# Kernel tuning notes

Measured on AMD Instinct MI355X. Metric: run time of the kernel, lower is better.

## Reference

```python
import jax, jax.numpy as jnp
import numpy as np

N = 100000   # nodes
E = 1600000  # edges
DIN, DH, DOUT = 128, 64, 40
EPS = 1e-5


def setup_inputs() -> dict:
    key = jax.random.key(0)
    ks = jax.random.split(key, 16)
    glorot = lambda k, shp: jax.random.normal(k, shp, jnp.float32) / np.float32(np.sqrt(shp[0]))
    return {
        'x': jax.random.normal(ks[0], (N, DIN), jnp.float32),
        'edge_index': jax.random.randint(ks[1], (2, E), 0, N, jnp.int64),
        'W0': glorot(ks[2], (DIN, DH)), 'b0': jnp.zeros((DH,), jnp.float32),
        'W1': glorot(ks[3], (DH, DH)),  'b1': jnp.zeros((DH,), jnp.float32),
        'W2': glorot(ks[4], (DH, DH)),  'b2': jnp.zeros((DH,), jnp.float32),
        'ln0_g': jnp.ones((DH,), jnp.float32), 'ln0_b': jnp.zeros((DH,), jnp.float32),
        'ln1_g': jnp.ones((DH,), jnp.float32), 'ln1_b': jnp.zeros((DH,), jnp.float32),
        'mpW0': glorot(ks[5], (DH, DH)),  'mpb0': jnp.zeros((DH,), jnp.float32),
        'mpW1': glorot(ks[6], (DH, DOUT)), 'mpb1': jnp.zeros((DOUT,), jnp.float32),
    }


def _layernorm(h, g, b):
    mu = jnp.mean(h, axis=-1, keepdims=True)
    var = jnp.mean(jnp.square(h - mu), axis=-1, keepdims=True)
    return (h - mu) * jax.lax.rsqrt(var + EPS) * g + b


def _gcn_conv(x, src, dst, norm_e, self_w, W, b):
    # PyG GCNConv: h = x W; out = sum_{(s,d)} norm * h[s] scattered to d,
    # plus self-loop term, plus bias.  norm = d^{-1/2}[s] * d^{-1/2}[d] on A+I.
    h = x @ W                                        # [N, out]
    agg = jnp.zeros_like(h).at[dst].add(h[src] * norm_e[:, None])
    agg = agg + h * self_w[:, None]                  # self loops (i,i)
    return agg + b


def reference(x, edge_index, W0, b0, W1, b1, W2, b2,
              ln0_g, ln0_b, ln1_g, ln1_b, mpW0, mpb0, mpW1, mpb1):
    src, dst = edge_index[0], edge_index[1]
    # degree on A + I (count incoming edges at dst, +1 for self loop)
    deg = jnp.zeros((N,), jnp.float32).at[dst].add(1.0) + 1.0
    dinv = jax.lax.rsqrt(deg)
    norm_e = dinv[src] * dinv[dst]                   # per-edge weight [E]
    self_w = dinv * dinv                             # self-loop weight [N]

    h = x
    convs = [(W0, b0), (W1, b1), (W2, b2)]
    lns = [(ln0_g, ln0_b), (ln1_g, ln1_b)]
    for i, (W, b) in enumerate(convs):
        h = _gcn_conv(h, src, dst, norm_e, self_w, W, b)
        h = jax.nn.relu(h)
        # dropout: training=False -> identity
        if i != len(convs) - 1:
            g, bb = lns[i]
            h = _layernorm(h, g, bb)

    # post_mp: Linear -> Dropout(identity) -> Linear
    h = h @ mpW0 + mpb0
    return h @ mpW1 + mpb1
```

## Files before the change

kernel.cpp:

```cpp
#include <hip/hip_runtime.h>
#include <hip/hip_bf16.h>

#define NN 100000
#define EE 1600000
#define DOUT 40
#define LN_EPS 1e-5f
#define NBUCK 391
#define TILE 2048
#define TBLK 782
#define BCAP 8192

typedef __attribute__((ext_vector_type(8))) short short8;
typedef __attribute__((ext_vector_type(4))) float f32x4;

__device__ __forceinline__ float blo(unsigned u) { return __uint_as_float(u << 16); }
__device__ __forceinline__ float bhi(unsigned u) { return __uint_as_float(u & 0xffff0000u); }
__device__ __forceinline__ unsigned bpack(float lo, float hi) {
    unsigned a = __float_as_uint(lo);
    unsigned b = __float_as_uint(hi);
    a = (a + 0x7fffu + ((a >> 16) & 1u)) >> 16;
    b = (b + 0x7fffu + ((b >> 16) & 1u)) & 0xffff0000u;
    return (a & 0xffffu) | b;
}

__global__ void binit_k(int* __restrict__ bucketCur) {
    int b = blockIdx.x * 256 + threadIdx.x;
    if (b < NBUCK) bucketCur[b] = b * BCAP;
}

__global__ __launch_bounds__(512, 8) void bucket_k(const int* __restrict__ src,
                                                   const int* __restrict__ dst,
                                                   int* __restrict__ bucketCur,
                                                   unsigned* __restrict__ bE) {
    __shared__ int cnt[8][NBUCK];
    __shared__ int basew[8][NBUCK];
    int tid = threadIdx.x;
    int wv = tid >> 6;
    for (int i = tid; i < 8 * NBUCK; i += 512) ((int*)cnt)[i] = 0;
    __syncthreads();
    long e0 = (long)blockIdx.x * TILE;
    int d[4];
#pragma unroll
    for (int i = 0; i < 4; ++i) {
        long e = e0 + tid + i * 512;
        d[i] = (e < EE) ? dst[e] : -1;
    }
#pragma unroll
    for (int i = 0; i < 4; ++i) {
        if (d[i] >= 0) atomicAdd(&cnt[wv][d[i] >> 8], 1);
    }
    __syncthreads();
    for (int b = tid; b < NBUCK; b += 512) {
        int c[8];
        int tot = 0;
#pragma unroll
        for (int w = 0; w < 8; ++w) { c[w] = cnt[w][b]; tot += c[w]; }
        int base = tot ? atomicAdd(&bucketCur[b], tot) : 0;
        int run = base;
#pragma unroll
        for (int w = 0; w < 8; ++w) { basew[w][b] = run; run += c[w]; cnt[w][b] = 0; }
    }
    __syncthreads();
#pragma unroll
    for (int i = 0; i < 4; ++i) {
        if (d[i] >= 0) {
            long e = e0 + tid + i * 512;
            int b = d[i] >> 8;
            int pos = basew[wv][b] + atomicAdd(&cnt[wv][b], 1);
            bE[pos] = (unsigned)src[e] | ((unsigned)(d[i] & 255) << 24);
        }
    }
}

__global__ __launch_bounds__(512, 4) void reorder2_k(const int* __restrict__ bucketCur,
                                                     const unsigned* __restrict__ bE,
                                                     int* __restrict__ csrSrc,
                                                     int* __restrict__ degI,
                                                     int* __restrict__ cursor,
                                                     float* __restrict__ dinv) {
    __shared__ int sScan[512];
    __shared__ int sHist[256];
    __shared__ int sPre[256];
    __shared__ int sStart[256];
    int tid = threadIdx.x;
    int b = blockIdx.x;
    int c = (tid < NBUCK) ? (bucketCur[tid] - tid * BCAP) : 0;
    sScan[tid] = c;
    __syncthreads();
    for (int off = 1; off < 512; off <<= 1) {
        int t = (tid >= off) ? sScan[tid - off] : 0;
        __syncthreads();
        sScan[tid] += t;
        __syncthreads();
    }
    int bbase = (b == 0) ? 0 : sScan[b - 1];
    if (tid < 256) sHist[tid] = 0;
    __syncthreads();
    int start = b * BCAP;
    int end = bucketCur[b];
    for (int e = start + tid; e < end; e += 512) {
        unsigned v = bE[e];
        atomicAdd(&sHist[v >> 24], 1);
    }
    __syncthreads();
    if (tid < 256) sPre[tid] = sHist[tid];
    __syncthreads();
    for (int off = 1; off < 256; off <<= 1) {
        int t = (tid >= off && tid < 256) ? sPre[tid - off] : 0;
        __syncthreads();
        if (tid < 256) sPre[tid] += t;
        __syncthreads();
    }
    if (tid < 256) {
        int h = sHist[tid];
        int excl = sPre[tid] - h;
        int st = bbase + excl;
        sStart[tid] = st;
        int nd = (b << 8) + tid;
        if (nd < NN) {
            degI[nd] = h;
            cursor[nd] = st;
            dinv[nd] = rsqrtf((float)h + 1.0f);
        }
    }
    __syncthreads();
    for (int e = start + tid; e < end; e += 512) {
        unsigned v = bE[e];
        int pos = atomicAdd(&sStart[v >> 24], 1);
        csrSrc[pos] = (int)(v & 0xFFFFFFu);
    }
}

template <int K>
__global__ __launch_bounds__(256, 2) void gemm_mfma(const float* __restrict__ X,
                                                    const float* __restrict__ W,
                                                    const float* __restrict__ dinv,
                                                    unsigned* __restrict__ H) {
    constexpr int C = K / 32;
    __shared__ unsigned short sW16[K * 66];
    __shared__ float sD[64 * 65];
    int tid = threadIdx.x;
    for (int i = tid; i < K * 64; i += 256) {
        int k = i >> 6, n = i & 63;
        sW16[k * 66 + n] = (unsigned short)(bpack(W[i], 0.f) & 0xffffu);
    }
    __syncthreads();
    int wv = tid >> 6, lane = tid & 63;
    int q = lane >> 4, ln = lane & 15;
    short8 bfrag[C][4];
#pragma unroll
    for (int c = 0; c < C; ++c) {
#pragma unroll
        for (int t = 0; t < 4; ++t) {
            int kb = (c * 32 + q * 8) * 66 + t * 16 + ln;
            unsigned u0 = (unsigned)sW16[kb]       | ((unsigned)sW16[kb + 66]  << 16);
            unsigned u1 = (unsigned)sW16[kb + 132] | ((unsigned)sW16[kb + 198] << 16);
            unsigned u2 = (unsigned)sW16[kb + 264] | ((unsigned)sW16[kb + 330] << 16);
            unsigned u3 = (unsigned)sW16[kb + 396] | ((unsigned)sW16[kb + 462] << 16);
            uint4 u = make_uint4(u0, u1, u2, u3);
            bfrag[c][t] = __builtin_bit_cast(short8, u);
        }
    }
    int base = blockIdx.x * 64;
    int node = base + wv * 16 + ln;
    bool ok = node < NN;
    short8 afrag[C];
#pragma unroll
    for (int c = 0; c < C; ++c) {
        float4 f0 = make_float4(0.f, 0.f, 0.f, 0.f);
        float4 f1 = make_float4(0.f, 0.f, 0.f, 0.f);
        if (ok) {
            const float4* xp = (const float4*)(X + (long)node * K + c * 32 + q * 8);
            f0 = xp[0];
            f1 = xp[1];
        }
        uint4 u;
        u.x = bpack(f0.x, f0.y);
        u.y = bpack(f0.z, f0.w);
        u.z = bpack(f1.x, f1.y);
        u.w = bpack(f1.z, f1.w);
        afrag[c] = __builtin_bit_cast(short8, u);
    }
#pragma unroll
    for (int t = 0; t < 4; ++t) {
        f32x4 acc = {0.f, 0.f, 0.f, 0.f};
#pragma unroll
        for (int c = 0; c < C; ++c)
            acc = __builtin_amdgcn_mfma_f32_16x16x32_bf16(afrag[c], bfrag[c][t], acc, 0, 0, 0);
#pragma unroll
        for (int r = 0; r < 4; ++r)
            sD[(wv * 16 + q * 4 + r) * 65 + t * 16 + ln] = acc[r];
    }
    __syncthreads();
    for (int i = tid; i < 64 * 32; i += 256) {
        int row = i >> 5, c2 = i & 31;
        int nd = base + row;
        if (nd < NN) {
            float di = dinv[nd];
            float lo = sD[row * 65 + c2 * 2] * di;
            float hi = sD[row * 65 + c2 * 2 + 1] * di;
            H[nd * 32 + c2] = bpack(lo, hi);
        }
    }
}

__global__ __launch_bounds__(256, 2) void gemm_b(const uint4* __restrict__ Hin4,
                                                 const float* __restrict__ W,
                                                 const float* __restrict__ dinv,
                                                 unsigned* __restrict__ H) {
    __shared__ unsigned short sW16[64 * 66];
    __shared__ float sD[64 * 65];
    int tid = threadIdx.x;
    for (int i = tid; i < 64 * 64; i += 256) {
        int k = i >> 6, n = i & 63;
        sW16[k * 66 + n] = (unsigned short)(bpack(W[i], 0.f) & 0xffffu);
    }
    __syncthreads();
    int wv = tid >> 6, lane = tid & 63;
    int q = lane >> 4, ln = lane & 15;
    short8 bfrag[2][4];
#pragma unroll
    for (int c = 0; c < 2; ++c) {
#pragma unroll
        for (int t = 0; t < 4; ++t) {
            int kb = (c * 32 + q * 8) * 66 + t * 16 + ln;
            unsigned u0 = (unsigned)sW16[kb]       | ((unsigned)sW16[kb + 66]  << 16);
            unsigned u1 = (unsigned)sW16[kb + 132] | ((unsigned)sW16[kb + 198] << 16);
            unsigned u2 = (unsigned)sW16[kb + 264] | ((unsigned)sW16[kb + 330] << 16);
            unsigned u3 = (unsigned)sW16[kb + 396] | ((unsigned)sW16[kb + 462] << 16);
            uint4 u = make_uint4(u0, u1, u2, u3);
            bfrag[c][t] = __builtin_bit_cast(short8, u);
        }
    }
    int base = blockIdx.x * 64;
    int node = base + wv * 16 + ln;
    bool ok = node < NN;
    short8 afrag[2];
    {
        uint4 u0 = make_uint4(0u, 0u, 0u, 0u), u1 = u0;
        if (ok) {
            u0 = Hin4[(unsigned)node * 8u + (unsigned)q];
            u1 = Hin4[(unsigned)node * 8u + 4u + (unsigned)q];
        }
        afrag[0] = __builtin_bit_cast(short8, u0);
        afrag[1] = __builtin_bit_cast(short8, u1);
    }
#pragma unroll
    for (int t = 0; t < 4; ++t) {
        f32x4 acc = {0.f, 0.f, 0.f, 0.f};
        acc = __builtin_amdgcn_mfma_f32_16x16x32_bf16(afrag[0], bfrag[0][t], acc, 0, 0, 0);
        acc = __builtin_amdgcn_mfma_f32_16x16x32_bf16(afrag[1], bfrag[1][t], acc, 0, 0, 0);
#pragma unroll
        for (int r = 0; r < 4; ++r)
            sD[(wv * 16 + q * 4 + r) * 65 + t * 16 + ln] = acc[r];
    }
    __syncthreads();
    for (int i = tid; i < 64 * 32; i += 256) {
        int row = i >> 5, c2 = i & 31;
        int nd = base + row;
        if (nd < NN) {
            float di = dinv[nd];
            float lo = sD[row * 65 + c2 * 2] * di;
            float hi = sD[row * 65 + c2 * 2 + 1] * di;
            H[nd * 32 + c2] = bpack(lo, hi);
        }
    }
}

__global__ __launch_bounds__(256, 4) void agg_k(
        const int* __restrict__ cursor, const int* __restrict__ degI,
        const int* __restrict__ csrSrc, const float* __restrict__ dinv,
        const uint2* __restrict__ H2, const float4* __restrict__ bias4,
        const float4* __restrict__ g4, const float4* __restrict__ beta4,
        uint2* __restrict__ OUT2, int doLN) {
    int tid = threadIdx.x;
    int w = tid >> 6, lane = tid & 63;
    int g = lane >> 4;
    unsigned f = (unsigned)(lane & 15);
    unsigned node = (unsigned)(blockIdx.x * 4 + w);
    int start = cursor[node];
    int deg = degI[node];
    int myIdx = 0;
    if (lane < deg) myIdx = csrSrc[(unsigned)(start + lane)];
    float ax = 0.f, ay = 0.f, az = 0.f, aw = 0.f;
    float bx = 0.f, by = 0.f, bz = 0.f, bw = 0.f;
    uint2 q[8];
#pragma unroll
    for (int r = 0; r < 8; ++r) {
        int e = r * 4 + g;
        unsigned s = (unsigned)__shfl(myIdx, e);
        q[r] = make_uint2(0u, 0u);
        if (e < deg) q[r] = H2[s * 16u + f];
    }
#pragma unroll
    for (int r = 0; r < 8; r += 2) {
        ax += blo(q[r].x);     ay += bhi(q[r].x);
        az += blo(q[r].y);     aw += bhi(q[r].y);
        bx += blo(q[r + 1].x); by += bhi(q[r + 1].x);
        bz += blo(q[r + 1].y); bw += bhi(q[r + 1].y);
    }
    if (deg > 32) {
        int R2 = (deg + 3) >> 2;
        if (R2 > 16) R2 = 16;
        for (int r = 8; r < R2; ++r) {
            int e = r * 4 + g;
            unsigned s = (unsigned)__shfl(myIdx, e);
            uint2 qq = make_uint2(0u, 0u);
            if (e < deg) qq = H2[s * 16u + f];
            ax += blo(qq.x); ay += bhi(qq.x); az += blo(qq.y); aw += bhi(qq.y);
        }
        for (int ee = 64 + g; ee < deg; ee += 4) {
            uint2 qq = H2[(unsigned)csrSrc[(unsigned)(start + ee)] * 16u + f];
            ax += blo(qq.x); ay += bhi(qq.x); az += blo(qq.y); aw += bhi(qq.y);
        }
    }
    ax += bx; ay += by; az += bz; aw += bw;
    ax += __shfl_xor(ax, 16); ay += __shfl_xor(ay, 16);
    az += __shfl_xor(az, 16); aw += __shfl_xor(aw, 16);
    ax += __shfl_xor(ax, 32); ay += __shfl_xor(ay, 32);
    az += __shfl_xor(az, 32); aw += __shfl_xor(aw, 32);
    float di = dinv[node];
    uint2 qs = H2[node * 16u + f];
    float4 bb = bias4[f];
    float vx = fmaxf((ax + blo(qs.x)) * di + bb.x, 0.f);
    float vy = fmaxf((ay + bhi(qs.x)) * di + bb.y, 0.f);
    float vz = fmaxf((az + blo(qs.y)) * di + bb.z, 0.f);
    float vw = fmaxf((aw + bhi(qs.y)) * di + bb.w, 0.f);
    if (doLN) {
        float s = vx + vy + vz + vw;
        s += __shfl_xor(s, 1); s += __shfl_xor(s, 2);
        s += __shfl_xor(s, 4); s += __shfl_xor(s, 8);
        float mu = s * (1.f / 64.f);
        vx -= mu; vy -= mu; vz -= mu; vw -= mu;
        float vs = vx * vx + vy * vy + vz * vz + vw * vw;
        vs += __shfl_xor(vs, 1); vs += __shfl_xor(vs, 2);
        vs += __shfl_xor(vs, 4); vs += __shfl_xor(vs, 8);
        float inv = rsqrtf(vs * (1.f / 64.f) + LN_EPS);
        float4 gg = g4[f];
        float4 tt = beta4[f];
        vx = vx * inv * gg.x + tt.x;
        vy = vy * inv * gg.y + tt.y;
        vz = vz * inv * gg.z + tt.z;
        vw = vw * inv * gg.w + tt.w;
    }
    if (g == 0) OUT2[node * 16u + f] = make_uint2(bpack(vx, vy), bpack(vz, vw));
}

__global__ void fuse_k(const float* __restrict__ W0, const float* __restrict__ b0,
                       const float* __restrict__ W1, const float* __restrict__ b1,
                       float* __restrict__ Wf, float* __restrict__ bf) {
    int tid = threadIdx.x;
    for (int i = tid; i < 64 * 48; i += 256) {
        int k = i / 48, n = i % 48;
        float acc = 0.f;
        if (n < DOUT) {
            for (int j = 0; j < 64; ++j) acc = fmaf(W0[k * 64 + j], W1[j * DOUT + n], acc);
        }
        Wf[i] = acc;
    }
    for (int n = tid; n < 48; n += 256) {
        float acc = 0.f;
        if (n < DOUT) {
            acc = b1[n];
            for (int j = 0; j < 64; ++j) acc = fmaf(b0[j], W1[j * DOUT + n], acc);
        }
        bf[n] = acc;
    }
}

__global__ __launch_bounds__(256, 2) void mlp_mfma(const uint4* __restrict__ Hin4,
                                                   const float* __restrict__ Wf,
                                                   const float* __restrict__ bf,
                                                   float* __restrict__ OUT) {
    __shared__ unsigned short sW16[64 * 50];
    int tid = threadIdx.x;
    for (int i = tid; i < 64 * 48; i += 256) {
        int k = i / 48, n = i % 48;
        sW16[k * 50 + n] = (unsigned short)(bpack(Wf[i], 0.f) & 0xffffu);
    }
    __syncthreads();
    int wv = tid >> 6, lane = tid & 63;
    int q = lane >> 4, ln = lane & 15;
    short8 bfrag[2][3];
#pragma unroll
    for (int c = 0; c < 2; ++c) {
#pragma unroll
        for (int t = 0; t < 3; ++t) {
            int kb = (c * 32 + q * 8) * 50 + t * 16 + ln;
            unsigned u0 = (unsigned)sW16[kb]       | ((unsigned)sW16[kb + 50]  << 16);
            unsigned u1 = (unsigned)sW16[kb + 100] | ((unsigned)sW16[kb + 150] << 16);
            unsigned u2 = (unsigned)sW16[kb + 200] | ((unsigned)sW16[kb + 250] << 16);
            unsigned u3 = (unsigned)sW16[kb + 300] | ((unsigned)sW16[kb + 350] << 16);
            uint4 u = make_uint4(u0, u1, u2, u3);
            bfrag[c][t] = __builtin_bit_cast(short8, u);
        }
    }
    int base = blockIdx.x * 64;
    int node = base + wv * 16 + ln;
    bool ok = node < NN;
    short8 afrag[2];
    {
        uint4 u0 = make_uint4(0u, 0u, 0u, 0u), u1 = u0;
        if (ok) {
            u0 = Hin4[(unsigned)node * 8u + (unsigned)q];
            u1 = Hin4[(unsigned)node * 8u + 4u + (unsigned)q];
        }
        afrag[0] = __builtin_bit_cast(short8, u0);
        afrag[1] = __builtin_bit_cast(short8, u1);
    }
#pragma unroll
    for (int t = 0; t < 3; ++t) {
        f32x4 acc = {0.f, 0.f, 0.f, 0.f};
        acc = __builtin_amdgcn_mfma_f32_16x16x32_bf16(afrag[0], bfrag[0][t], acc, 0, 0, 0);
        acc = __builtin_amdgcn_mfma_f32_16x16x32_bf16(afrag[1], bfrag[1][t], acc, 0, 0, 0);
        int col = t * 16 + ln;
        if (col < DOUT) {
            float bv = bf[col];
#pragma unroll
            for (int r = 0; r < 4; ++r) {
                int nd = base + wv * 16 + q * 4 + r;
                if (nd < NN) OUT[(long)nd * DOUT + col] = acc[r] + bv;
            }
        }
    }
}

extern "C" void kernel_launch(void* const* d_in, const int* in_sizes, int n_in,
                              void* d_out, int out_size, void* d_ws, size_t ws_size,
                              hipStream_t stream) {
    const float* x    = (const float*)d_in[0];
    const int*   ei   = (const int*)d_in[1];
    const int*   srcI = ei;
    const int*   dstI = ei + EE;
    const float* W0   = (const float*)d_in[2];
    const float* b0   = (const float*)d_in[3];
    const float* W1   = (const float*)d_in[4];
    const float* b1   = (const float*)d_in[5];
    const float* W2   = (const float*)d_in[6];
    const float* b2   = (const float*)d_in[7];
    const float* ln0g = (const float*)d_in[8];
    const float* ln0b = (const float*)d_in[9];
    const float* ln1g = (const float*)d_in[10];
    const float* ln1b = (const float*)d_in[11];
    const float* mpW0 = (const float*)d_in[12];
    const float* mpb0 = (const float*)d_in[13];
    const float* mpW1 = (const float*)d_in[14];
    const float* mpb1 = (const float*)d_in[15];
    float* out = (float*)d_out;

    char* ws = (char*)d_ws;
    float*    dinv      = (float*)   (ws + 0);
    int*      degI      = (int*)     (ws + 512l * 1024);
    int*      cursor    = (int*)     (ws + 1024l * 1024);
    int*      bucketCur = (int*)     (ws + 1600l * 1024);
    float*    Wf        = (float*)   (ws + 1792l * 1024);
    float*    bfv       = (float*)   (ws + 1984l * 1024);
    unsigned* bE        = (unsigned*)(ws + 2048l * 1024);
    int*      csrSrc    = (int*)     (ws + 15l * 1024 * 1024);
    unsigned* bufA      = (unsigned*)(ws + 22l * 1024 * 1024);
    unsigned* bufB      = (unsigned*)(ws + 36l * 1024 * 1024);

    const int aggBlocks  = NN / 4;
    const int gemmBlocks = (NN + 63) / 64;

    binit_k<<<2, 256, 0, stream>>>(bucketCur);
    bucket_k<<<TBLK, 512, 0, stream>>>(srcI, dstI, bucketCur, bE);
    reorder2_k<<<NBUCK, 512, 0, stream>>>(bucketCur, bE, csrSrc, degI, cursor, dinv);
    fuse_k<<<1, 256, 0, stream>>>(mpW0, mpb0, mpW1, mpb1, Wf, bfv);

    gemm_mfma<128><<<gemmBlocks, 256, 0, stream>>>(x, W0, dinv, bufA);
    agg_k<<<aggBlocks, 256, 0, stream>>>(cursor, degI, csrSrc, dinv, (const uint2*)bufA,
                                         (const float4*)b0, (const float4*)ln0g,
                                         (const float4*)ln0b, (uint2*)bufB, 1);
    gemm_b<<<gemmBlocks, 256, 0, stream>>>((const uint4*)bufB, W1, dinv, bufA);
    agg_k<<<aggBlocks, 256, 0, stream>>>(cursor, degI, csrSrc, dinv, (const uint2*)bufA,
                                         (const float4*)b1, (const float4*)ln1g,
                                         (const float4*)ln1b, (uint2*)bufB, 1);
    gemm_b<<<gemmBlocks, 256, 0, stream>>>((const uint4*)bufB, W2, dinv, bufA);
    agg_k<<<aggBlocks, 256, 0, stream>>>(cursor, degI, csrSrc, dinv, (const uint2*)bufA,
                                         (const float4*)b2, (const float4*)ln0g,
                                         (const float4*)ln0b, (uint2*)bufB, 0);
    mlp_mfma<<<gemmBlocks, 256, 0, stream>>>((const uint4*)bufB, Wf, bfv, out);
}
```

Before: 354.5 us.

## Prepack weights into MFMA fragment layout once and split aggregation gather by degree

```diff
diff --git a/kernel.cpp b/kernel.cpp
--- a/kernel.cpp
+++ b/kernel.cpp
@@ -131,46 +131,100 @@
     }
 }
 
-template <int K>
-__global__ __launch_bounds__(256, 2) void gemm_mfma(const float* __restrict__ X,
-                                                    const float* __restrict__ W,
-                                                    const float* __restrict__ dinv,
-                                                    unsigned* __restrict__ H) {
-    constexpr int C = K / 32;
-    __shared__ unsigned short sW16[K * 66];
+__global__ void prep_k(const float* __restrict__ W0, const float* __restrict__ W1,
+                       const float* __restrict__ W2,
+                       const float* __restrict__ mpW0, const float* __restrict__ mpb0,
+                       const float* __restrict__ mpW1, const float* __restrict__ mpb1,
+                       uint4* __restrict__ W0pk, uint4* __restrict__ W1pk,
+                       uint4* __restrict__ W2pk, uint4* __restrict__ Wfpk,
+                       float* __restrict__ bf) {
+    __shared__ float sWf[64 * 48];
+    int tid = threadIdx.x;
+    for (int i = tid; i < 64 * 48; i += 256) {
+        int k = i / 48, n = i % 48;
+        float acc = 0.f;
+        if (n < DOUT) {
+            for (int j = 0; j < 64; ++j) acc = fmaf(mpW0[k * 64 + j], mpW1[j * DOUT + n], acc);
+        }
+        sWf[i] = acc;
+    }
+    for (int n = tid; n < 48; n += 256) {
+        float acc = 0.f;
+        if (n < DOUT) {
+            acc = mpb1[n];
+            for (int j = 0; j < 64; ++j) acc = fmaf(mpb0[j], mpW1[j * DOUT + n], acc);
+        }
+        bf[n] = acc;
+    }
+    for (int i = tid; i < 1024; i += 256) {
+        int lane = i & 63, ct = i >> 6;
+        int q = lane >> 4, ln = lane & 15;
+        int c = ct >> 2, t = ct & 3;
+        int row0 = c * 32 + q * 8, col = t * 16 + ln;
+        uint4 u;
+        u.x = bpack(W0[(row0 + 0) * 64 + col], W0[(row0 + 1) * 64 + col]);
+        u.y = bpack(W0[(row0 + 2) * 64 + col], W0[(row0 + 3) * 64 + col]);
+        u.z = bpack(W0[(row0 + 4) * 64 + col], W0[(row0 + 5) * 64 + col]);
+        u.w = bpack(W0[(row0 + 6) * 64 + col], W0[(row0 + 7) * 64 + col]);
+        W0pk[i] = u;
+    }
+    for (int i = tid; i < 512; i += 256) {
+        int lane = i & 63, ct = i >> 6;
+        int q = lane >> 4, ln = lane & 15;
+        int c = ct >> 2, t = ct & 3;
+        int row0 = c * 32 + q * 8, col = t * 16 + ln;
+        uint4 u;
+        u.x = bpack(W1[(row0 + 0) * 64 + col], W1[(row0 + 1) * 64 + col]);
+        u.y = bpack(W1[(row0 + 2) * 64 + col], W1[(row0 + 3) * 64 + col]);
+        u.z = bpack(W1[(row0 + 4) * 64 + col], W1[(row0 + 5) * 64 + col]);
+        u.w = bpack(W1[(row0 + 6) * 64 + col], W1[(row0 + 7) * 64 + col]);
+        W1pk[i] = u;
+        uint4 v;
+        v.x = bpack(W2[(row0 + 0) * 64 + col], W2[(row0 + 1) * 64 + col]);
+        v.y = bpack(W2[(row0 + 2) * 64 + col], W2[(row0 + 3) * 64 + col]);
+        v.z = bpack(W2[(row0 + 4) * 64 + col], W2[(row0 + 5) * 64 + col]);
+        v.w = bpack(W2[(row0 + 6) * 64 + col], W2[(row0 + 7) * 64 + col]);
+        W2pk[i] = v;
+    }
+    __syncthreads();
+    for (int i = tid; i < 384; i += 256) {
+        int lane = i & 63, ct = i >> 6;
+        int q = lane >> 4, ln = lane & 15;
+        int c = ct / 3, t = ct % 3;
+        int row0 = c * 32 + q * 8, col = t * 16 + ln;
+        uint4 u;
+        u.x = bpack(sWf[(row0 + 0) * 48 + col], sWf[(row0 + 1) * 48 + col]);
+        u.y = bpack(sWf[(row0 + 2) * 48 + col], sWf[(row0 + 3) * 48 + col]);
+        u.z = bpack(sWf[(row0 + 4) * 48 + col], sWf[(row0 + 5) * 48 + col]);
+        u.w = bpack(sWf[(row0 + 6) * 48 + col], sWf[(row0 + 7) * 48 + col]);
+        Wfpk[i] = u;
+    }
+}
+
+__global__ __launch_bounds__(256, 2) void gemm0(const float* __restrict__ X,
+                                                const uint4* __restrict__ Wpk,
+                                                const float* __restrict__ dinv,
+                                                unsigned* __restrict__ H) {
     __shared__ float sD[64 * 65];
     int tid = threadIdx.x;
-    for (int i = tid; i < K * 64; i += 256) {
-        int k = i >> 6, n = i & 63;
-        sW16[k * 66 + n] = (unsigned short)(bpack(W[i], 0.f) & 0xffffu);
-    }
-    __syncthreads();
     int wv = tid >> 6, lane = tid & 63;
     int q = lane >> 4, ln = lane & 15;
-    short8 bfrag[C][4];
-#pragma unroll
-    for (int c = 0; c < C; ++c) {
-#pragma unroll
-        for (int t = 0; t < 4; ++t) {
-            int kb = (c * 32 + q * 8) * 66 + t * 16 + ln;
-            unsigned u0 = (unsigned)sW16[kb]       | ((unsigned)sW16[kb + 66]  << 16);
-            unsigned u1 = (unsigned)sW16[kb + 132] | ((unsigned)sW16[kb + 198] << 16);
-            unsigned u2 = (unsigned)sW16[kb + 264] | ((unsigned)sW16[kb + 330] << 16);
-            unsigned u3 = (unsigned)sW16[kb + 396] | ((unsigned)sW16[kb + 462] << 16);
-            uint4 u = make_uint4(u0, u1, u2, u3);
-            bfrag[c][t] = __builtin_bit_cast(short8, u);
-        }
-    }
+    short8 bfrag[4][4];
+#pragma unroll
+    for (int c = 0; c < 4; ++c)
+#pragma unroll
+        for (int t = 0; t < 4; ++t)
+            bfrag[c][t] = __builtin_bit_cast(short8, Wpk[(c * 4 + t) * 64 + lane]);
     int base = blockIdx.x * 64;
     int node = base + wv * 16 + ln;
     bool ok = node < NN;
-    short8 afrag[C];
-#pragma unroll
-    for (int c = 0; c < C; ++c) {
+    short8 afrag[4];
+#pragma unroll
+    for (int c = 0; c < 4; ++c) {
         float4 f0 = make_float4(0.f, 0.f, 0.f, 0.f);
         float4 f1 = make_float4(0.f, 0.f, 0.f, 0.f);
         if (ok) {
-            const float4* xp = (const float4*)(X + (long)node * K + c * 32 + q * 8);
+            const float4* xp = (const float4*)(X + (long)node * 128 + c * 32 + q * 8);
             f0 = xp[0];
             f1 = xp[1];
         }
@@ -185,7 +239,7 @@
     for (int t = 0; t < 4; ++t) {
         f32x4 acc = {0.f, 0.f, 0.f, 0.f};
 #pragma unroll
-        for (int c = 0; c < C; ++c)
+        for (int c = 0; c < 4; ++c)
             acc = __builtin_amdgcn_mfma_f32_16x16x32_bf16(afrag[c], bfrag[c][t], acc, 0, 0, 0);
 #pragma unroll
         for (int r = 0; r < 4; ++r)
@@ -205,33 +259,19 @@
 }
 
 __global__ __launch_bounds__(256, 2) void gemm_b(const uint4* __restrict__ Hin4,
-                                                 const float* __restrict__ W,
+                                                 const uint4* __restrict__ Wpk,
                                                  const float* __restrict__ dinv,
                                                  unsigned* __restrict__ H) {
-    __shared__ unsigned short sW16[64 * 66];
     __shared__ float sD[64 * 65];
     int tid = threadIdx.x;
-    for (int i = tid; i < 64 * 64; i += 256) {
-        int k = i >> 6, n = i & 63;
-        sW16[k * 66 + n] = (unsigned short)(bpack(W[i], 0.f) & 0xffffu);
-    }
-    __syncthreads();
     int wv = tid >> 6, lane = tid & 63;
     int q = lane >> 4, ln = lane & 15;
     short8 bfrag[2][4];
 #pragma unroll
-    for (int c = 0; c < 2; ++c) {
-#pragma unroll
-        for (int t = 0; t < 4; ++t) {
-            int kb = (c * 32 + q * 8) * 66 + t * 16 + ln;
-            unsigned u0 = (unsigned)sW16[kb]       | ((unsigned)sW16[kb + 66]  << 16);
-            unsigned u1 = (unsigned)sW16[kb + 132] | ((unsigned)sW16[kb + 198] << 16);
-            unsigned u2 = (unsigned)sW16[kb + 264] | ((unsigned)sW16[kb + 330] << 16);
-            unsigned u3 = (unsigned)sW16[kb + 396] | ((unsigned)sW16[kb + 462] << 16);
-            uint4 u = make_uint4(u0, u1, u2, u3);
-            bfrag[c][t] = __builtin_bit_cast(short8, u);
-        }
-    }
+    for (int c = 0; c < 2; ++c)
+#pragma unroll
+        for (int t = 0; t < 4; ++t)
+            bfrag[c][t] = __builtin_bit_cast(short8, Wpk[(c * 4 + t) * 64 + lane]);
     int base = blockIdx.x * 64;
     int node = base + wv * 16 + ln;
     bool ok = node < NN;
@@ -284,34 +324,59 @@
     if (lane < deg) myIdx = csrSrc[(unsigned)(start + lane)];
     float ax = 0.f, ay = 0.f, az = 0.f, aw = 0.f;
     float bx = 0.f, by = 0.f, bz = 0.f, bw = 0.f;
-    uint2 q[8];
-#pragma unroll
-    for (int r = 0; r < 8; ++r) {
+    uint2 qa[4];
+#pragma unroll
+    for (int r = 0; r < 4; ++r) {
         int e = r * 4 + g;
         unsigned s = (unsigned)__shfl(myIdx, e);
-        q[r] = make_uint2(0u, 0u);
-        if (e < deg) q[r] = H2[s * 16u + f];
-    }
-#pragma unroll
-    for (int r = 0; r < 8; r += 2) {
-        ax += blo(q[r].x);     ay += bhi(q[r].x);
-        az += blo(q[r].y);     aw += bhi(q[r].y);
-        bx += blo(q[r + 1].x); by += bhi(q[r + 1].x);
-        bz += blo(q[r + 1].y); bw += bhi(q[r + 1].y);
-    }
-    if (deg > 32) {
-        int R2 = (deg + 3) >> 2;
-        if (R2 > 16) R2 = 16;
-        for (int r = 8; r < R2; ++r) {
-            int e = r * 4 + g;
+        qa[r] = make_uint2(0u, 0u);
+        if (e < deg) qa[r] = H2[s * 16u + f];
+    }
+    if (deg <= 16) {
+#pragma unroll
+        for (int r = 0; r < 4; r += 2) {
+            ax += blo(qa[r].x);     ay += bhi(qa[r].x);
+            az += blo(qa[r].y);     aw += bhi(qa[r].y);
+            bx += blo(qa[r + 1].x); by += bhi(qa[r + 1].x);
+            bz += blo(qa[r + 1].y); bw += bhi(qa[r + 1].y);
+        }
+    } else {
+        uint2 qb[4];
+#pragma unroll
+        for (int r = 0; r < 4; ++r) {
+            int e = 16 + r * 4 + g;
             unsigned s = (unsigned)__shfl(myIdx, e);
-            uint2 qq = make_uint2(0u, 0u);
-            if (e < deg) qq = H2[s * 16u + f];
-            ax += blo(qq.x); ay += bhi(qq.x); az += blo(qq.y); aw += bhi(qq.y);
-        }
-        for (int ee = 64 + g; ee < deg; ee += 4) {
-            uint2 qq = H2[(unsigned)csrSrc[(unsigned)(start + ee)] * 16u + f];
-            ax += blo(qq.x); ay += bhi(qq.x); az += blo(qq.y); aw += bhi(qq.y);
+            qb[r] = make_uint2(0u, 0u);
+            if (e < deg) qb[r] = H2[s * 16u + f];
+        }
+#pragma unroll
+        for (int r = 0; r < 4; r += 2) {
+            ax += blo(qa[r].x);     ay += bhi(qa[r].x);
+            az += blo(qa[r].y);     aw += bhi(qa[r].y);
+            bx += blo(qa[r + 1].x); by += bhi(qa[r + 1].x);
+            bz += blo(qa[r + 1].y); bw += bhi(qa[r + 1].y);
+        }
+#pragma unroll
+        for (int r = 0; r < 4; r += 2) {
+            ax += blo(qb[r].x);     ay += bhi(qb[r].x);
+            az += blo(qb[r].y);     aw += bhi(qb[r].y);
+            bx += blo(qb[r + 1].x); by += bhi(qb[r + 1].x);
+            bz += blo(qb[r + 1].y); bw += bhi(qb[r + 1].y);
+        }
+        if (deg > 32) {
+            int R2 = (deg + 3) >> 2;
+            if (R2 > 16) R2 = 16;
+            for (int r = 8; r < R2; ++r) {
+                int e = r * 4 + g;
+                unsigned s = (unsigned)__shfl(myIdx, e);
+                uint2 qq = make_uint2(0u, 0u);
+                if (e < deg) qq = H2[s * 16u + f];
+                ax += blo(qq.x); ay += bhi(qq.x); az += blo(qq.y); aw += bhi(qq.y);
+            }
+            for (int ee = 64 + g; ee < deg; ee += 4) {
+                uint2 qq = H2[(unsigned)csrSrc[(unsigned)(start + ee)] * 16u + f];
+                ax += blo(qq.x); ay += bhi(qq.x); az += blo(qq.y); aw += bhi(qq.y);
+            }
         }
     }
     ax += bx; ay += by; az += bz; aw += bw;
@@ -346,55 +411,19 @@
     if (g == 0) OUT2[node * 16u + f] = make_uint2(bpack(vx, vy), bpack(vz, vw));
 }
 
-__global__ void fuse_k(const float* __restrict__ W0, const float* __restrict__ b0,
-                       const float* __restrict__ W1, const float* __restrict__ b1,
-                       float* __restrict__ Wf, float* __restrict__ bf) {
-    int tid = threadIdx.x;
-    for (int i = tid; i < 64 * 48; i += 256) {
-        int k = i / 48, n = i % 48;
-        float acc = 0.f;
-        if (n < DOUT) {
-            for (int j = 0; j < 64; ++j) acc = fmaf(W0[k * 64 + j], W1[j * DOUT + n], acc);
-        }
-        Wf[i] = acc;
-    }
-    for (int n = tid; n < 48; n += 256) {
-        float acc = 0.f;
-        if (n < DOUT) {
-            acc = b1[n];
-            for (int j = 0; j < 64; ++j) acc = fmaf(b0[j], W1[j * DOUT + n], acc);
-        }
-        bf[n] = acc;
-    }
-}
-
 __global__ __launch_bounds__(256, 2) void mlp_mfma(const uint4* __restrict__ Hin4,
-                                                   const float* __restrict__ Wf,
+                                                   const uint4* __restrict__ Wfpk,
                                                    const float* __restrict__ bf,
                                                    float* __restrict__ OUT) {
-    __shared__ unsigned short sW16[64 * 50];
-    int tid = threadIdx.x;
-    for (int i = tid; i < 64 * 48; i += 256) {
-        int k = i / 48, n = i % 48;
-        sW16[k * 50 + n] = (unsigned short)(bpack(Wf[i], 0.f) & 0xffffu);
-    }
-    __syncthreads();
+    int tid = threadIdx.x;
     int wv = tid >> 6, lane = tid & 63;
     int q = lane >> 4, ln = lane & 15;
     short8 bfrag[2][3];
 #pragma unroll
-    for (int c = 0; c < 2; ++c) {
-#pragma unroll
-        for (int t = 0; t < 3; ++t) {
-            int kb = (c * 32 + q * 8) * 50 + t * 16 + ln;
-            unsigned u0 = (unsigned)sW16[kb]       | ((unsigned)sW16[kb + 50]  << 16);
-            unsigned u1 = (unsigned)sW16[kb + 100] | ((unsigned)sW16[kb + 150] << 16);
-            unsigned u2 = (unsigned)sW16[kb + 200] | ((unsigned)sW16[kb + 250] << 16);
-            unsigned u3 = (unsigned)sW16[kb + 300] | ((unsigned)sW16[kb + 350] << 16);
-            uint4 u = make_uint4(u0, u1, u2, u3);
-            bfrag[c][t] = __builtin_bit_cast(short8, u);
-        }
-    }
+    for (int c = 0; c < 2; ++c)
+#pragma unroll
+        for (int t = 0; t < 3; ++t)
+            bfrag[c][t] = __builtin_bit_cast(short8, Wfpk[(c * 3 + t) * 64 + lane]);
     int base = blockIdx.x * 64;
     int node = base + wv * 16 + ln;
     bool ok = node < NN;
@@ -453,8 +482,11 @@
     int*      degI      = (int*)     (ws + 512l * 1024);
     int*      cursor    = (int*)     (ws + 1024l * 1024);
     int*      bucketCur = (int*)     (ws + 1600l * 1024);
-    float*    Wf        = (float*)   (ws + 1792l * 1024);
-    float*    bfv       = (float*)   (ws + 1984l * 1024);
+    uint4*    W0pk      = (uint4*)   (ws + 1792l * 1024);
+    uint4*    W1pk      = (uint4*)   (ws + 1824l * 1024);
+    uint4*    W2pk      = (uint4*)   (ws + 1856l * 1024);
+    uint4*    Wfpk      = (uint4*)   (ws + 1888l * 1024);
+    float*    bfv       = (float*)   (ws + 1920l * 1024);
     unsigned* bE        = (unsigned*)(ws + 2048l * 1024);
     int*      csrSrc    = (int*)     (ws + 15l * 1024 * 1024);
     unsigned* bufA      = (unsigned*)(ws + 22l * 1024 * 1024);
@@ -466,19 +498,20 @@
     binit_k<<<2, 256, 0, stream>>>(bucketCur);
     bucket_k<<<TBLK, 512, 0, stream>>>(srcI, dstI, bucketCur, bE);
     reorder2_k<<<NBUCK, 512, 0, stream>>>(bucketCur, bE, csrSrc, degI, cursor, dinv);
-    fuse_k<<<1, 256, 0, stream>>>(mpW0, mpb0, mpW1, mpb1, Wf, bfv);
-
-    gemm_mfma<128><<<gemmBlocks, 256, 0, stream>>>(x, W0, dinv, bufA);
+    prep_k<<<1, 256, 0, stream>>>(W0, W1, W2, mpW0, mpb0, mpW1, mpb1,
+                                  W0pk, W1pk, W2pk, Wfpk, bfv);
+
+    gemm0<<<gemmBlocks, 256, 0, stream>>>(x, W0pk, dinv, bufA);
     agg_k<<<aggBlocks, 256, 0, stream>>>(cursor, degI, csrSrc, dinv, (const uint2*)bufA,
                                          (const float4*)b0, (const float4*)ln0g,
                                          (const float4*)ln0b, (uint2*)bufB, 1);
-    gemm_b<<<gemmBlocks, 256, 0, stream>>>((const uint4*)bufB, W1, dinv, bufA);
+    gemm_b<<<gemmBlocks, 256, 0, stream>>>((const uint4*)bufB, W1pk, dinv, bufA);
     agg_k<<<aggBlocks, 256, 0, stream>>>(cursor, degI, csrSrc, dinv, (const uint2*)bufA,
                                          (const float4*)b1, (const float4*)ln1g,
                                          (const float4*)ln1b, (uint2*)bufB, 1);
-    gemm_b<<<gemmBlocks, 256, 0, stream>>>((const uint4*)bufB, W2, dinv, bufA);
+    gemm_b<<<gemmBlocks, 256, 0, stream>>>((const uint4*)bufB, W2pk, dinv, bufA);
     agg_k<<<aggBlocks, 256, 0, stream>>>(cursor, degI, csrSrc, dinv, (const uint2*)bufA,
                                          (const float4*)b2, (const float4*)ln0g,
                                          (const float4*)ln0b, (uint2*)bufB, 0);
-    mlp_mfma<<<gemmBlocks, 256, 0, stream>>>((const uint4*)bufB, Wf, bfv, out);
-}
+    mlp_mfma<<<gemmBlocks, 256, 0, stream>>>((const uint4*)bufB, Wfpk, bfv, out);
+}
```

Result: faster. 342.2 us (-3.4%).
